# Optimization experiments

Measured on AMD Instinct MI355X. Metric: run time of the kernel, lower is better.

The kernel has to match this reference:

```python
import jax, jax.numpy as jnp
import numpy as np
import math

B, S, H, D = 4, 4096, 2048, 128  # batch, seq_len, hidden_dim, head_size

def setup_inputs() -> dict:
    key = jax.random.key(0)
    ks = jax.random.split(key, 7)
    scale = 1.0 / math.sqrt(H)
    return {
        "x": jax.random.normal(ks[0], (B, S, H), dtype=jnp.float32),
        "Wq": jax.random.normal(ks[1], (H, D), dtype=jnp.float32) * scale,
        "bq": jnp.zeros((D,), dtype=jnp.float32),
        "Wk": jax.random.normal(ks[2], (H, D), dtype=jnp.float32) * scale,
        "bk": jnp.zeros((D,), dtype=jnp.float32),
        "Wv": jax.random.normal(ks[3], (H, D), dtype=jnp.float32) * scale,
        "bv": jnp.zeros((D,), dtype=jnp.float32),
    }

def reference(x, Wq, bq, Wk, bk, Wv, bv):
    # projections: [B,S,D]
    q = x @ Wq + bq
    k = x @ Wk + bk
    v = x @ Wv + bv
    # raw scores [B,S,S] with causal mask, NO pre-softmax scaling (as in source)
    scores = jnp.einsum('bsd,btd->bst', q, k)
    causal = jnp.tril(jnp.ones((S, S), dtype=bool))
    scores = jnp.where(causal, scores, -jnp.inf)
    # non-standard: scale AFTER softmax by 1/sqrt(head_size)
    w = jax.nn.softmax(scores, axis=-1) * (1.0 / math.sqrt(D))
    # dropout p=0.0 -> identity
    return jnp.einsum('bst,btd->bsd', w, v)
```

## Files before the change

kernel.cpp:

```cpp
#include <hip/hip_runtime.h>
#include <math.h>
#include <stdint.h>

#define SEQ   4096
#define HID   2048
#define HD    128
#define NROWS 16384

typedef __attribute__((ext_vector_type(8))) short bf16x8;
typedef __attribute__((ext_vector_type(4))) float f32x4;

static constexpr float OSCALE = 0.088388347648318447f;

using gvptr = const __attribute__((address_space(1))) void*;
using lvptr = __attribute__((address_space(3))) void*;
__device__ __forceinline__ void gld_lds16(const void* g, void* l) {
    __builtin_amdgcn_global_load_lds((gvptr)g, (lvptr)l, 16, 0, 0);
}

__device__ __forceinline__ unsigned short f2bf_rne(float f) {
    union { float f; unsigned u; } v; v.f = f;
    unsigned u = v.u + 0x7fffu + ((v.u >> 16) & 1u);
    return (unsigned short)(u >> 16);
}
__device__ __forceinline__ unsigned short f2bf_tr(float f) {
    union { float f; unsigned u; } v; v.f = f;
    return (unsigned short)(v.u >> 16);
}
__device__ __forceinline__ float bf2f(unsigned short h) {
    union { unsigned u; float f; } v; v.u = ((unsigned)h) << 16;
    return v.f;
}

__global__ __launch_bounds__(256) void prep_w(
    const float* __restrict__ Wq, const float* __restrict__ Wk, const float* __restrict__ Wv,
    unsigned short* __restrict__ wth, unsigned short* __restrict__ wtl)
{
    __shared__ float T[64][68];
    const int tid = threadIdx.x;
    const int k0 = blockIdx.x * 64, n0 = blockIdx.y * 64, mm = blockIdx.z;
    const float* W = (mm == 0) ? Wq : (mm == 1) ? Wk : Wv;
    #pragma unroll
    for (int i = 0; i < 4; ++i) {
        const int fi = i * 256 + tid, kk = fi >> 4, nc = (fi & 15) * 4;
        const float4 w = *(const float4*)(W + (size_t)(k0 + kk) * HD + n0 + nc);
        T[kk][nc] = w.x; T[kk][nc + 1] = w.y; T[kk][nc + 2] = w.z; T[kk][nc + 3] = w.w;
    }
    __syncthreads();
    unsigned short* oh = wth + (size_t)mm * HD * HID;
    unsigned short* ol = wtl + (size_t)mm * HD * HID;
    #pragma unroll
    for (int i = 0; i < 4; ++i) {
        const int fi = i * 256 + tid, nn = fi >> 4, kc = (fi & 15) * 4;
        const float a = T[kc][nn], b = T[kc + 1][nn], c = T[kc + 2][nn], d = T[kc + 3][nn];
        ushort4 hv, lv;
        hv.x = f2bf_rne(a); hv.y = f2bf_rne(b); hv.z = f2bf_rne(c); hv.w = f2bf_rne(d);
        lv.x = f2bf_rne(a - bf2f(hv.x)); lv.y = f2bf_rne(b - bf2f(hv.y));
        lv.z = f2bf_rne(c - bf2f(hv.z)); lv.w = f2bf_rne(d - bf2f(hv.w));
        *(ushort4*)(oh + (size_t)(n0 + nn) * HID + k0 + kc) = hv;
        *(ushort4*)(ol + (size_t)(n0 + nn) * HID + k0 + kc) = lv;
    }
}

__global__ __launch_bounds__(256, 2) void qkv_fused(
    const float* __restrict__ x,
    const float* __restrict__ bq, const float* __restrict__ bk, const float* __restrict__ bv,
    const unsigned short* __restrict__ wth, const unsigned short* __restrict__ wtl,
    unsigned short* __restrict__ qh, unsigned short* __restrict__ ql,
    unsigned short* __restrict__ kh, unsigned short* __restrict__ kl,
    unsigned short* __restrict__ vth)
{
    __shared__ unsigned short Ah[64][72], Al[64][72];
    __shared__ unsigned short Bt[5][64][64];

    const int tid = threadIdx.x, wave = tid >> 6, lane = tid & 63;
    const int l15 = lane & 15, q4 = lane >> 4;
    const int wr = wave >> 1, wc = wave & 1;
    const int r0 = (blockIdx.x >> 1) * 64;
    const int hc = blockIdx.x & 1;

    const unsigned short* wsrc[5] = {
        wth + (size_t)hc * 64 * HID,
        wtl + (size_t)hc * 64 * HID,
        wth + (size_t)HD * HID + (size_t)hc * 64 * HID,
        wtl + (size_t)HD * HID + (size_t)hc * 64 * HID,
        wth + (size_t)2 * HD * HID + (size_t)hc * 64 * HID };

    const int srow_off = lane >> 3;
    const int schunk   = ((lane & 7) ^ (lane >> 3)) * 8;

    f32x4 accq[2][2], acck[2][2], accv[2][2];
    #pragma unroll
    for (int i = 0; i < 2; ++i)
        #pragma unroll
        for (int j = 0; j < 2; ++j) {
            accq[i][j] = (f32x4){0.f, 0.f, 0.f, 0.f};
            acck[i][j] = (f32x4){0.f, 0.f, 0.f, 0.f};
            accv[i][j] = (f32x4){0.f, 0.f, 0.f, 0.f};
        }

    const float* xbase = x + (size_t)r0 * HID;

    float4 xv[4];
    #pragma unroll
    for (int i = 0; i < 4; ++i) {
        const int fi = i * 256 + tid, row = fi >> 4, kc = (fi & 15) * 4;
        xv[i] = *(const float4*)(xbase + (size_t)row * HID + kc);
    }

    for (int k0 = 0; k0 < HID; k0 += 64) {
        __syncthreads();
        {
            #pragma unroll
            for (int a = 0; a < 5; ++a) {
                #pragma unroll
                for (int c = 0; c < 2; ++c) {
                    const int row = wave * 16 + c * 8 + srow_off;
                    gld_lds16(wsrc[a] + (size_t)row * HID + k0 + schunk,
                              &Bt[a][wave * 16 + c * 8][0]);
                }
            }
        }
        #pragma unroll
        for (int i = 0; i < 4; ++i) {
            const int fi = i * 256 + tid, row = fi >> 4, kc = (fi & 15) * 4;
            ushort4 hv, lv;
            hv.x = f2bf_tr(xv[i].x); hv.y = f2bf_tr(xv[i].y);
            hv.z = f2bf_tr(xv[i].z); hv.w = f2bf_tr(xv[i].w);
            lv.x = f2bf_tr(xv[i].x - bf2f(hv.x)); lv.y = f2bf_tr(xv[i].y - bf2f(hv.y));
            lv.z = f2bf_tr(xv[i].z - bf2f(hv.z)); lv.w = f2bf_tr(xv[i].w - bf2f(hv.w));
            *(ushort4*)&Ah[row][kc] = hv;
            *(ushort4*)&Al[row][kc] = lv;
        }
        __syncthreads();

        const int kn = (k0 + 64 < HID) ? (k0 + 64) : 0;
        #pragma unroll
        for (int i = 0; i < 4; ++i) {
            const int fi = i * 256 + tid, row = fi >> 4, kc = (fi & 15) * 4;
            xv[i] = *(const float4*)(xbase + (size_t)row * HID + kn + kc);
        }

        #pragma unroll
        for (int ks = 0; ks < 2; ++ks) {
            bf16x8 ah[2], al[2];
            #pragma unroll
            for (int mt = 0; mt < 2; ++mt) {
                ah[mt] = *(const bf16x8*)&Ah[wr * 32 + mt * 16 + l15][ks * 32 + q4 * 8];
                al[mt] = *(const bf16x8*)&Al[wr * 32 + mt * 16 + l15][ks * 32 + q4 * 8];
            }
            const int pc = ((ks * 4 + q4) ^ (l15 & 7)) * 8;
            #pragma unroll
            for (int nt = 0; nt < 2; ++nt) {
                const int br = wc * 32 + nt * 16 + l15;
                const bf16x8 qbh = *(const bf16x8*)&Bt[0][br][pc];
                const bf16x8 qbl = *(const bf16x8*)&Bt[1][br][pc];
                #pragma unroll
                for (int mt = 0; mt < 2; ++mt) {
                    accq[mt][nt] = __builtin_amdgcn_mfma_f32_16x16x32_bf16(ah[mt], qbh, accq[mt][nt], 0, 0, 0);
                    accq[mt][nt] = __builtin_amdgcn_mfma_f32_16x16x32_bf16(ah[mt], qbl, accq[mt][nt], 0, 0, 0);
                    accq[mt][nt] = __builtin_amdgcn_mfma_f32_16x16x32_bf16(al[mt], qbh, accq[mt][nt], 0, 0, 0);
                }
                const bf16x8 kbh = *(const bf16x8*)&Bt[2][br][pc];
                const bf16x8 kbl = *(const bf16x8*)&Bt[3][br][pc];
                #pragma unroll
                for (int mt = 0; mt < 2; ++mt) {
                    acck[mt][nt] = __builtin_amdgcn_mfma_f32_16x16x32_bf16(ah[mt], kbh, acck[mt][nt], 0, 0, 0);
                    acck[mt][nt] = __builtin_amdgcn_mfma_f32_16x16x32_bf16(ah[mt], kbl, acck[mt][nt], 0, 0, 0);
                    acck[mt][nt] = __builtin_amdgcn_mfma_f32_16x16x32_bf16(al[mt], kbh, acck[mt][nt], 0, 0, 0);
                }
                const bf16x8 vbh = *(const bf16x8*)&Bt[4][br][pc];
                #pragma unroll
                for (int mt = 0; mt < 2; ++mt)
                    accv[mt][nt] = __builtin_amdgcn_mfma_f32_16x16x32_bf16(ah[mt], vbh, accv[mt][nt], 0, 0, 0);
            }
        }
    }

    #pragma unroll
    for (int nt = 0; nt < 2; ++nt) {
        const int col = hc * 64 + wc * 32 + nt * 16 + l15;
        const float bbq = bq[col], bbk = bk[col], bbv = bv[col];
        #pragma unroll
        for (int mt = 0; mt < 2; ++mt) {
            const int Rb = r0 + wr * 32 + mt * 16 + q4 * 4;
            #pragma unroll
            for (int r = 0; r < 4; ++r) {
                const float vq = accq[mt][nt][r] + bbq;
                const unsigned short hq = f2bf_rne(vq);
                qh[(size_t)(Rb + r) * HD + col] = hq;
                ql[(size_t)(Rb + r) * HD + col] = f2bf_rne(vq - bf2f(hq));
                const float vk = acck[mt][nt][r] + bbk;
                const unsigned short hk = f2bf_rne(vk);
                kh[(size_t)(Rb + r) * HD + col] = hk;
                kl[(size_t)(Rb + r) * HD + col] = f2bf_rne(vk - bf2f(hk));
            }
            const int bi = Rb >> 12, s0 = Rb & 4095;
            ushort4 pv;
            pv.x = f2bf_rne(accv[mt][nt][0] + bbv);
            pv.y = f2bf_rne(accv[mt][nt][1] + bbv);
            pv.z = f2bf_rne(accv[mt][nt][2] + bbv);
            pv.w = f2bf_rne(accv[mt][nt][3] + bbv);
            *(ushort4*)(vth + ((size_t)(bi * HD + col)) * SEQ + s0) = pv;
        }
    }
}

__global__ __launch_bounds__(256, 2) void flash_mfma(
    const unsigned short* __restrict__ qh, const unsigned short* __restrict__ ql,
    const unsigned short* __restrict__ kh, const unsigned short* __restrict__ kl,
    const unsigned short* __restrict__ vth,
    unsigned short* __restrict__ oPb, float* __restrict__ mP, float* __restrict__ lP)
{
    __shared__ unsigned short Kh[64][128], Kl[64][128];
    __shared__ unsigned short Vt[128][64];
    __shared__ unsigned short Ps[4][16][72];

    const int tid = threadIdx.x, wave = tid >> 6, lane = tid & 63;
    const int l15 = lane & 15, q4 = lane >> 4;
    const int h = blockIdx.x & 3, pair = (blockIdx.x >> 2) & 31, b = blockIdx.x >> 7;

    const int krow_l = lane >> 4;
    const int vrow_l = lane >> 3;
    const int vsc = ((lane & 7) ^ (vrow_l & 7)) * 8;
    const int kkey7 = l15 & 7;
    const int vkey7 = l15 & 7;

    for (int side = 0; side < 2; ++side) {
        const int tt = side ? (63 - pair) : pair;
        const int n = tt + 1;
        const int j0 = (n * h) >> 2, j1 = (n * (h + 1)) >> 2;

        const int qrow = b * SEQ + tt * 64 + wave * 16 + l15;
        bf16x8 aqh[4], aql[4];
        #pragma unroll
        for (int ks = 0; ks < 4; ++ks) {
            aqh[ks] = *(const bf16x8*)(qh + (size_t)qrow * HD + ks * 32 + q4 * 8);
            aql[ks] = *(const bf16x8*)(ql + (size_t)qrow * HD + ks * 32 + q4 * 8);
        }
        f32x4 oa[8];
        #pragma unroll
        for (int d = 0; d < 8; ++d) oa[d] = (f32x4){0.f, 0.f, 0.f, 0.f};
        float m_r[4] = {-INFINITY, -INFINITY, -INFINITY, -INFINITY};
        float l_r[4] = {0.f, 0.f, 0.f, 0.f};

        for (int j = j0; j < j1; ++j) {
            __syncthreads();
            {
                const size_t kb = (size_t)b * SEQ + j * 64;
                #pragma unroll
                for (int c = 0; c < 4; ++c) {
                    const int rl = c * 4 + krow_l;
                    const int sc = (l15 ^ (rl & 7)) * 8;
                    const size_t gr = (kb + wave * 16 + rl) * HD + sc;
                    gld_lds16(kh + gr, &Kh[wave * 16 + c * 4][0]);
                    gld_lds16(kl + gr, &Kl[wave * 16 + c * 4][0]);
                }
                #pragma unroll
                for (int c = 0; c < 4; ++c)
                    gld_lds16(vth + ((size_t)(b * HD + wave * 32 + c * 8 + vrow_l)) * SEQ
                                  + j * 64 + vsc,
                              &Vt[wave * 32 + c * 8][0]);
            }
            __syncthreads();

            f32x4 s[4];
            #pragma unroll
            for (int nt = 0; nt < 4; ++nt) s[nt] = (f32x4){0.f, 0.f, 0.f, 0.f};
            #pragma unroll
            for (int ks = 0; ks < 4; ++ks) {
                const int pc = ((ks * 4 + q4) ^ kkey7) * 8;
                #pragma unroll
                for (int nt = 0; nt < 4; ++nt) {
                    const bf16x8 bh = *(const bf16x8*)&Kh[nt * 16 + l15][pc];
                    const bf16x8 bl = *(const bf16x8*)&Kl[nt * 16 + l15][pc];
                    s[nt] = __builtin_amdgcn_mfma_f32_16x16x32_bf16(aqh[ks], bh, s[nt], 0, 0, 0);
                    s[nt] = __builtin_amdgcn_mfma_f32_16x16x32_bf16(aql[ks], bh, s[nt], 0, 0, 0);
                    s[nt] = __builtin_amdgcn_mfma_f32_16x16x32_bf16(aqh[ks], bl, s[nt], 0, 0, 0);
                }
            }
            if (j == tt) {
                #pragma unroll
                for (int nt = 0; nt < 4; ++nt) {
                    const int cl = nt * 16 + l15;
                    #pragma unroll
                    for (int r = 0; r < 4; ++r) {
                        const int rl = wave * 16 + q4 * 4 + r;
                        if (cl > rl) s[nt][r] = -INFINITY;
                    }
                }
            }
            #pragma unroll
            for (int r = 0; r < 4; ++r) {
                float mt = fmaxf(fmaxf(s[0][r], s[1][r]), fmaxf(s[2][r], s[3][r]));
                mt = fmaxf(mt, __shfl_xor(mt, 1));
                mt = fmaxf(mt, __shfl_xor(mt, 2));
                mt = fmaxf(mt, __shfl_xor(mt, 4));
                mt = fmaxf(mt, __shfl_xor(mt, 8));
                const float mn = fmaxf(m_r[r], mt);
                const float al = __expf(m_r[r] - mn);
                m_r[r] = mn;
                const float p0 = __expf(s[0][r] - mn), p1 = __expf(s[1][r] - mn);
                const float p2 = __expf(s[2][r] - mn), p3 = __expf(s[3][r] - mn);
                Ps[wave][q4 * 4 + r][l15]      = f2bf_tr(p0);
                Ps[wave][q4 * 4 + r][16 + l15] = f2bf_tr(p1);
                Ps[wave][q4 * 4 + r][32 + l15] = f2bf_tr(p2);
                Ps[wave][q4 * 4 + r][48 + l15] = f2bf_tr(p3);
                float ps = p0 + p1 + p2 + p3;
                ps += __shfl_xor(ps, 1); ps += __shfl_xor(ps, 2);
                ps += __shfl_xor(ps, 4); ps += __shfl_xor(ps, 8);
                l_r[r] = l_r[r] * al + ps;
                #pragma unroll
                for (int d = 0; d < 8; ++d) oa[d][r] *= al;
            }
            const bf16x8 ap0 = *(const bf16x8*)&Ps[wave][l15][q4 * 8];
            const bf16x8 ap1 = *(const bf16x8*)&Ps[wave][l15][32 + q4 * 8];
            #pragma unroll
            for (int d = 0; d < 8; ++d) {
                const bf16x8 bv0 = *(const bf16x8*)&Vt[d * 16 + l15][(q4 ^ vkey7) * 8];
                const bf16x8 bv1 = *(const bf16x8*)&Vt[d * 16 + l15][((4 + q4) ^ vkey7) * 8];
                oa[d] = __builtin_amdgcn_mfma_f32_16x16x32_bf16(ap0, bv0, oa[d], 0, 0, 0);
                oa[d] = __builtin_amdgcn_mfma_f32_16x16x32_bf16(ap1, bv1, oa[d], 0, 0, 0);
            }
        }

        const int R0 = b * SEQ + tt * 64 + wave * 16 + q4 * 4;
        unsigned short* op = oPb + (size_t)h * NROWS * HD;
        #pragma unroll
        for (int d = 0; d < 8; ++d)
            #pragma unroll
            for (int r = 0; r < 4; ++r)
                op[(size_t)(R0 + r) * HD + d * 16 + l15] = f2bf_rne(oa[d][r]);
        if (l15 == 0) {
            #pragma unroll
            for (int r = 0; r < 4; ++r) {
                mP[h * NROWS + R0 + r] = m_r[r];
                lP[h * NROWS + R0 + r] = l_r[r];
            }
        }
    }
}

__global__ __launch_bounds__(256) void flash_merge(
    const unsigned short* __restrict__ oPb, const float* __restrict__ mP,
    const float* __restrict__ lP, float* __restrict__ out)
{
    const int idx = blockIdx.x * 256 + threadIdx.x;
    const int r = idx >> 5, c = (idx & 31) * 4;
    float m[4], l[4];
    #pragma unroll
    for (int i = 0; i < 4; ++i) { m[i] = mP[i * NROWS + r]; l[i] = lP[i * NROWS + r]; }
    float M = fmaxf(fmaxf(m[0], m[1]), fmaxf(m[2], m[3]));
    float a[4], lsum = 0.f;
    #pragma unroll
    for (int i = 0; i < 4; ++i) { a[i] = __expf(m[i] - M); lsum += l[i] * a[i]; }
    const float inv = OSCALE / lsum;
    float ox = 0.f, oy = 0.f, oz = 0.f, ow = 0.f;
    #pragma unroll
    for (int i = 0; i < 4; ++i) {
        const ushort4 ov = *(const ushort4*)(oPb + (size_t)i * NROWS * HD + (size_t)r * HD + c);
        ox += a[i] * bf2f(ov.x); oy += a[i] * bf2f(ov.y);
        oz += a[i] * bf2f(ov.z); ow += a[i] * bf2f(ov.w);
    }
    float4 o; o.x = ox * inv; o.y = oy * inv; o.z = oz * inv; o.w = ow * inv;
    *(float4*)(out + (size_t)r * HD + c) = o;
}

extern "C" void kernel_launch(void* const* d_in, const int* in_sizes, int n_in,
                              void* d_out, int out_size, void* d_ws, size_t ws_size,
                              hipStream_t stream)
{
    (void)in_sizes; (void)n_in; (void)out_size; (void)ws_size;
    const float* x  = (const float*)d_in[0];
    const float* Wq = (const float*)d_in[1];
    const float* bq = (const float*)d_in[2];
    const float* Wk = (const float*)d_in[3];
    const float* bk = (const float*)d_in[4];
    const float* Wv = (const float*)d_in[5];
    const float* bv = (const float*)d_in[6];
    float* out = (float*)d_out;

    char* w = (char*)d_ws;
    unsigned short* qh  = (unsigned short*)(w);
    unsigned short* ql  = (unsigned short*)(w + 4194304);
    unsigned short* kh  = (unsigned short*)(w + 8388608);
    unsigned short* kl  = (unsigned short*)(w + 12582912);
    unsigned short* vth = (unsigned short*)(w + 16777216);
    unsigned short* wth = (unsigned short*)(w + 20971520);
    unsigned short* wtl = (unsigned short*)(w + 22544384);
    unsigned short* oPb = (unsigned short*)(w + 24117248);
    float* mP = (float*)(w + 40894464);
    float* lP = (float*)(w + 41156608);

    prep_w<<<dim3(32, 2, 3), 256, 0, stream>>>(Wq, Wk, Wv, wth, wtl);
    qkv_fused<<<512, 256, 0, stream>>>(x, bq, bk, bv, wth, wtl, qh, ql, kh, kl, vth);
    flash_mfma<<<512, 256, 0, stream>>>(qh, ql, kh, kl, vth, oPb, mP, lP);
    flash_merge<<<2048, 256, 0, stream>>>(oPb, mP, lP, out);
}
```

Before: 320.7 us.

## Load QKV weight fragments directly into registers and retile waves by column

The QKV projection kernel no longer stages the five weight tiles through shared memory with global_load_lds. Each wave now owns a 16-column slice across all 64 rows and loads its B fragments straight from global memory into registers. The A fragments are still read from shared memory for four row tiles. This removes the LDS weight buffer and the LDS reads of B, which frees shared memory and may raise occupancy. In exchange, the per-lane global loads are strided by HID with no coalescing across lanes, and each wave now issues more A-fragment LDS reads.

Result: slower. 339.2 us (+5.8%).

```diff
diff --git a/kernel.cpp b/kernel.cpp
--- a/kernel.cpp
+++ b/kernel.cpp
@@ -71,33 +71,27 @@
     unsigned short* __restrict__ vth)
 {
     __shared__ unsigned short Ah[64][72], Al[64][72];
-    __shared__ unsigned short Bt[5][64][64];
 
     const int tid = threadIdx.x, wave = tid >> 6, lane = tid & 63;
     const int l15 = lane & 15, q4 = lane >> 4;
-    const int wr = wave >> 1, wc = wave & 1;
     const int r0 = (blockIdx.x >> 1) * 64;
     const int hc = blockIdx.x & 1;
 
-    const unsigned short* wsrc[5] = {
-        wth + (size_t)hc * 64 * HID,
-        wtl + (size_t)hc * 64 * HID,
-        wth + (size_t)HD * HID + (size_t)hc * 64 * HID,
-        wtl + (size_t)HD * HID + (size_t)hc * 64 * HID,
-        wth + (size_t)2 * HD * HID + (size_t)hc * 64 * HID };
-
-    const int srow_off = lane >> 3;
-    const int schunk   = ((lane & 7) ^ (lane >> 3)) * 8;
-
-    f32x4 accq[2][2], acck[2][2], accv[2][2];
-    #pragma unroll
-    for (int i = 0; i < 2; ++i)
-        #pragma unroll
-        for (int j = 0; j < 2; ++j) {
-            accq[i][j] = (f32x4){0.f, 0.f, 0.f, 0.f};
-            acck[i][j] = (f32x4){0.f, 0.f, 0.f, 0.f};
-            accv[i][j] = (f32x4){0.f, 0.f, 0.f, 0.f};
-        }
+    const int col = hc * 64 + wave * 16 + l15;
+    const unsigned short* pQh = wth + (size_t)col * HID;
+    const unsigned short* pQl = wtl + (size_t)col * HID;
+    const unsigned short* pKh = pQh + (size_t)HD * HID;
+    const unsigned short* pKl = pQl + (size_t)HD * HID;
+    const unsigned short* pVh = pKh + (size_t)HD * HID;
+    const int kq = q4 * 8;
+
+    f32x4 accq[4], acck[4], accv[4];
+    #pragma unroll
+    for (int mt = 0; mt < 4; ++mt) {
+        accq[mt] = (f32x4){0.f, 0.f, 0.f, 0.f};
+        acck[mt] = (f32x4){0.f, 0.f, 0.f, 0.f};
+        accv[mt] = (f32x4){0.f, 0.f, 0.f, 0.f};
+    }
 
     const float* xbase = x + (size_t)r0 * HID;
 
@@ -110,17 +104,18 @@
 
     for (int k0 = 0; k0 < HID; k0 += 64) {
         __syncthreads();
-        {
-            #pragma unroll
-            for (int a = 0; a < 5; ++a) {
-                #pragma unroll
-                for (int c = 0; c < 2; ++c) {
-                    const int row = wave * 16 + c * 8 + srow_off;
-                    gld_lds16(wsrc[a] + (size_t)row * HID + k0 + schunk,
-                              &Bt[a][wave * 16 + c * 8][0]);
-                }
-            }
-        }
+
+        const bf16x8 b0qh = *(const bf16x8*)(pQh + k0 + kq);
+        const bf16x8 b0ql = *(const bf16x8*)(pQl + k0 + kq);
+        const bf16x8 b0kh = *(const bf16x8*)(pKh + k0 + kq);
+        const bf16x8 b0kl = *(const bf16x8*)(pKl + k0 + kq);
+        const bf16x8 b0vh = *(const bf16x8*)(pVh + k0 + kq);
+        const bf16x8 b1qh = *(const bf16x8*)(pQh + k0 + 32 + kq);
+        const bf16x8 b1ql = *(const bf16x8*)(pQl + k0 + 32 + kq);
+        const bf16x8 b1kh = *(const bf16x8*)(pKh + k0 + 32 + kq);
+        const bf16x8 b1kl = *(const bf16x8*)(pKl + k0 + 32 + kq);
+        const bf16x8 b1vh = *(const bf16x8*)(pVh + k0 + 32 + kq);
+
         #pragma unroll
         for (int i = 0; i < 4; ++i) {
             const int fi = i * 256 + tid, row = fi >> 4, kc = (fi & 15) * 4;
@@ -141,68 +136,61 @@
             xv[i] = *(const float4*)(xbase + (size_t)row * HID + kn + kc);
         }
 
-        #pragma unroll
-        for (int ks = 0; ks < 2; ++ks) {
-            bf16x8 ah[2], al[2];
-            #pragma unroll
-            for (int mt = 0; mt < 2; ++mt) {
-                ah[mt] = *(const bf16x8*)&Ah[wr * 32 + mt * 16 + l15][ks * 32 + q4 * 8];
-                al[mt] = *(const bf16x8*)&Al[wr * 32 + mt * 16 + l15][ks * 32 + q4 * 8];
-            }
-            const int pc = ((ks * 4 + q4) ^ (l15 & 7)) * 8;
-            #pragma unroll
-            for (int nt = 0; nt < 2; ++nt) {
-                const int br = wc * 32 + nt * 16 + l15;
-                const bf16x8 qbh = *(const bf16x8*)&Bt[0][br][pc];
-                const bf16x8 qbl = *(const bf16x8*)&Bt[1][br][pc];
-                #pragma unroll
-                for (int mt = 0; mt < 2; ++mt) {
-                    accq[mt][nt] = __builtin_amdgcn_mfma_f32_16x16x32_bf16(ah[mt], qbh, accq[mt][nt], 0, 0, 0);
-                    accq[mt][nt] = __builtin_amdgcn_mfma_f32_16x16x32_bf16(ah[mt], qbl, accq[mt][nt], 0, 0, 0);
-                    accq[mt][nt] = __builtin_amdgcn_mfma_f32_16x16x32_bf16(al[mt], qbh, accq[mt][nt], 0, 0, 0);
-                }
-                const bf16x8 kbh = *(const bf16x8*)&Bt[2][br][pc];
-                const bf16x8 kbl = *(const bf16x8*)&Bt[3][br][pc];
-                #pragma unroll
-                for (int mt = 0; mt < 2; ++mt) {
-                    acck[mt][nt] = __builtin_amdgcn_mfma_f32_16x16x32_bf16(ah[mt], kbh, acck[mt][nt], 0, 0, 0);
-                    acck[mt][nt] = __builtin_amdgcn_mfma_f32_16x16x32_bf16(ah[mt], kbl, acck[mt][nt], 0, 0, 0);
-                    acck[mt][nt] = __builtin_amdgcn_mfma_f32_16x16x32_bf16(al[mt], kbh, acck[mt][nt], 0, 0, 0);
-                }
-                const bf16x8 vbh = *(const bf16x8*)&Bt[4][br][pc];
-                #pragma unroll
-                for (int mt = 0; mt < 2; ++mt)
-                    accv[mt][nt] = __builtin_amdgcn_mfma_f32_16x16x32_bf16(ah[mt], vbh, accv[mt][nt], 0, 0, 0);
-            }
-        }
-    }
-
-    #pragma unroll
-    for (int nt = 0; nt < 2; ++nt) {
-        const int col = hc * 64 + wc * 32 + nt * 16 + l15;
-        const float bbq = bq[col], bbk = bk[col], bbv = bv[col];
-        #pragma unroll
-        for (int mt = 0; mt < 2; ++mt) {
-            const int Rb = r0 + wr * 32 + mt * 16 + q4 * 4;
-            #pragma unroll
-            for (int r = 0; r < 4; ++r) {
-                const float vq = accq[mt][nt][r] + bbq;
-                const unsigned short hq = f2bf_rne(vq);
-                qh[(size_t)(Rb + r) * HD + col] = hq;
-                ql[(size_t)(Rb + r) * HD + col] = f2bf_rne(vq - bf2f(hq));
-                const float vk = acck[mt][nt][r] + bbk;
-                const unsigned short hk = f2bf_rne(vk);
-                kh[(size_t)(Rb + r) * HD + col] = hk;
-                kl[(size_t)(Rb + r) * HD + col] = f2bf_rne(vk - bf2f(hk));
-            }
-            const int bi = Rb >> 12, s0 = Rb & 4095;
-            ushort4 pv;
-            pv.x = f2bf_rne(accv[mt][nt][0] + bbv);
-            pv.y = f2bf_rne(accv[mt][nt][1] + bbv);
-            pv.z = f2bf_rne(accv[mt][nt][2] + bbv);
-            pv.w = f2bf_rne(accv[mt][nt][3] + bbv);
-            *(ushort4*)(vth + ((size_t)(bi * HD + col)) * SEQ + s0) = pv;
-        }
+        bf16x8 ah[4], al[4];
+        #pragma unroll
+        for (int mt = 0; mt < 4; ++mt) {
+            ah[mt] = *(const bf16x8*)&Ah[mt * 16 + l15][kq];
+            al[mt] = *(const bf16x8*)&Al[mt * 16 + l15][kq];
+        }
+        #pragma unroll
+        for (int mt = 0; mt < 4; ++mt) {
+            accq[mt] = __builtin_amdgcn_mfma_f32_16x16x32_bf16(ah[mt], b0qh, accq[mt], 0, 0, 0);
+            accq[mt] = __builtin_amdgcn_mfma_f32_16x16x32_bf16(ah[mt], b0ql, accq[mt], 0, 0, 0);
+            accq[mt] = __builtin_amdgcn_mfma_f32_16x16x32_bf16(al[mt], b0qh, accq[mt], 0, 0, 0);
+            acck[mt] = __builtin_amdgcn_mfma_f32_16x16x32_bf16(ah[mt], b0kh, acck[mt], 0, 0, 0);
+            acck[mt] = __builtin_amdgcn_mfma_f32_16x16x32_bf16(ah[mt], b0kl, acck[mt], 0, 0, 0);
+            acck[mt] = __builtin_amdgcn_mfma_f32_16x16x32_bf16(al[mt], b0kh, acck[mt], 0, 0, 0);
+            accv[mt] = __builtin_amdgcn_mfma_f32_16x16x32_bf16(ah[mt], b0vh, accv[mt], 0, 0, 0);
+        }
+        #pragma unroll
+        for (int mt = 0; mt < 4; ++mt) {
+            ah[mt] = *(const bf16x8*)&Ah[mt * 16 + l15][32 + kq];
+            al[mt] = *(const bf16x8*)&Al[mt * 16 + l15][32 + kq];
+        }
+        #pragma unroll
+        for (int mt = 0; mt < 4; ++mt) {
+            accq[mt] = __builtin_amdgcn_mfma_f32_16x16x32_bf16(ah[mt], b1qh, accq[mt], 0, 0, 0);
+            accq[mt] = __builtin_amdgcn_mfma_f32_16x16x32_bf16(ah[mt], b1ql, accq[mt], 0, 0, 0);
+            accq[mt] = __builtin_amdgcn_mfma_f32_16x16x32_bf16(al[mt], b1qh, accq[mt], 0, 0, 0);
+            acck[mt] = __builtin_amdgcn_mfma_f32_16x16x32_bf16(ah[mt], b1kh, acck[mt], 0, 0, 0);
+            acck[mt] = __builtin_amdgcn_mfma_f32_16x16x32_bf16(ah[mt], b1kl, acck[mt], 0, 0, 0);
+            acck[mt] = __builtin_amdgcn_mfma_f32_16x16x32_bf16(al[mt], b1kh, acck[mt], 0, 0, 0);
+            accv[mt] = __builtin_amdgcn_mfma_f32_16x16x32_bf16(ah[mt], b1vh, accv[mt], 0, 0, 0);
+        }
+    }
+
+    const float bbq = bq[col], bbk = bk[col], bbv = bv[col];
+    #pragma unroll
+    for (int mt = 0; mt < 4; ++mt) {
+        const int Rb = r0 + mt * 16 + q4 * 4;
+        #pragma unroll
+        for (int r = 0; r < 4; ++r) {
+            const float vq = accq[mt][r] + bbq;
+            const unsigned short hqv = f2bf_rne(vq);
+            qh[(size_t)(Rb + r) * HD + col] = hqv;
+            ql[(size_t)(Rb + r) * HD + col] = f2bf_rne(vq - bf2f(hqv));
+            const float vk = acck[mt][r] + bbk;
+            const unsigned short hkv = f2bf_rne(vk);
+            kh[(size_t)(Rb + r) * HD + col] = hkv;
+            kl[(size_t)(Rb + r) * HD + col] = f2bf_rne(vk - bf2f(hkv));
+        }
+        const int bi = Rb >> 12, s0 = Rb & 4095;
+        ushort4 pv;
+        pv.x = f2bf_rne(accv[mt][0] + bbv);
+        pv.y = f2bf_rne(accv[mt][1] + bbv);
+        pv.z = f2bf_rne(accv[mt][2] + bbv);
+        pv.w = f2bf_rne(accv[mt][3] + bbv);
+        *(ushort4*)(vth + ((size_t)(bi * HD + col)) * SEQ + s0) = pv;
     }
 }
 
```

## Split QKV projection into per-matrix blocks with full head width

Applied to the files above, without the earlier changes.

Replaces the fused QKV kernel, which computed half the head columns of Q, K and V together per block, with a kernel where each block computes all 128 columns of a single projection (Q, K or V) for a 64-row tile, launching 768 blocks. V blocks skip the low-part split of x and weights, so they do a third of the MFMA work and LDS loads of Q/K blocks. The x tile in LDS now uses an XOR swizzle instead of padding, and launch bounds ask for three blocks per CU. The trade-off is that each x tile is now read and converted by three blocks instead of two, and the uneven block costs may leave the load unbalanced.

Result: faster. 311.4 us (-2.9%).

```diff
diff --git a/kernel.cpp b/kernel.cpp
--- a/kernel.cpp
+++ b/kernel.cpp
@@ -62,7 +62,7 @@
     }
 }
 
-__global__ __launch_bounds__(256, 2) void qkv_fused(
+__global__ __launch_bounds__(256, 3) void qkv_split(
     const float* __restrict__ x,
     const float* __restrict__ bq, const float* __restrict__ bk, const float* __restrict__ bv,
     const unsigned short* __restrict__ wth, const unsigned short* __restrict__ wtl,
@@ -70,34 +70,29 @@
     unsigned short* __restrict__ kh, unsigned short* __restrict__ kl,
     unsigned short* __restrict__ vth)
 {
-    __shared__ unsigned short Ah[64][72], Al[64][72];
-    __shared__ unsigned short Bt[5][64][64];
+    __shared__ unsigned short Ah[64][64], Al[64][64];
+    __shared__ unsigned short Bh[128][64], Bl[128][64];
 
     const int tid = threadIdx.x, wave = tid >> 6, lane = tid & 63;
     const int l15 = lane & 15, q4 = lane >> 4;
     const int wr = wave >> 1, wc = wave & 1;
-    const int r0 = (blockIdx.x >> 1) * 64;
-    const int hc = blockIdx.x & 1;
-
-    const unsigned short* wsrc[5] = {
-        wth + (size_t)hc * 64 * HID,
-        wtl + (size_t)hc * 64 * HID,
-        wth + (size_t)HD * HID + (size_t)hc * 64 * HID,
-        wtl + (size_t)HD * HID + (size_t)hc * 64 * HID,
-        wth + (size_t)2 * HD * HID + (size_t)hc * 64 * HID };
-
-    const int srow_off = lane >> 3;
-    const int schunk   = ((lane & 7) ^ (lane >> 3)) * 8;
-
-    f32x4 accq[2][2], acck[2][2], accv[2][2];
-    #pragma unroll
-    for (int i = 0; i < 2; ++i)
-        #pragma unroll
-        for (int j = 0; j < 2; ++j) {
-            accq[i][j] = (f32x4){0.f, 0.f, 0.f, 0.f};
-            acck[i][j] = (f32x4){0.f, 0.f, 0.f, 0.f};
-            accv[i][j] = (f32x4){0.f, 0.f, 0.f, 0.f};
-        }
+    const int type = blockIdx.x % 3;
+    const int tile = blockIdx.x / 3;
+    const int r0 = tile * 64;
+    const bool qk = (type < 2);
+
+    const unsigned short* wh = wth + (size_t)type * HD * HID;
+    const unsigned short* wl = wtl + (size_t)type * HD * HID;
+
+    const int srow   = lane >> 3;
+    const int schunk = ((lane & 7) ^ srow) * 8;
+
+    f32x4 acc[2][4];
+    #pragma unroll
+    for (int mt = 0; mt < 2; ++mt)
+        #pragma unroll
+        for (int nt = 0; nt < 4; ++nt)
+            acc[mt][nt] = (f32x4){0.f, 0.f, 0.f, 0.f};
 
     const float* xbase = x + (size_t)r0 * HID;
 
@@ -110,27 +105,35 @@
 
     for (int k0 = 0; k0 < HID; k0 += 64) {
         __syncthreads();
+
         {
             #pragma unroll
-            for (int a = 0; a < 5; ++a) {
-                #pragma unroll
-                for (int c = 0; c < 2; ++c) {
-                    const int row = wave * 16 + c * 8 + srow_off;
-                    gld_lds16(wsrc[a] + (size_t)row * HID + k0 + schunk,
-                              &Bt[a][wave * 16 + c * 8][0]);
+            for (int c = 0; c < 4; ++c) {
+                const int row = wave * 32 + c * 8;
+                gld_lds16(wh + (size_t)(row + srow) * HID + k0 + schunk, &Bh[row][0]);
+            }
+            if (qk) {
+                #pragma unroll
+                for (int c = 0; c < 4; ++c) {
+                    const int row = wave * 32 + c * 8;
+                    gld_lds16(wl + (size_t)(row + srow) * HID + k0 + schunk, &Bl[row][0]);
                 }
             }
         }
         #pragma unroll
         for (int i = 0; i < 4; ++i) {
             const int fi = i * 256 + tid, row = fi >> 4, kc = (fi & 15) * 4;
-            ushort4 hv, lv;
+            const int pk = ((kc >> 3) ^ (row & 7)) * 8 + (kc & 7);
+            ushort4 hv;
             hv.x = f2bf_tr(xv[i].x); hv.y = f2bf_tr(xv[i].y);
             hv.z = f2bf_tr(xv[i].z); hv.w = f2bf_tr(xv[i].w);
-            lv.x = f2bf_tr(xv[i].x - bf2f(hv.x)); lv.y = f2bf_tr(xv[i].y - bf2f(hv.y));
-            lv.z = f2bf_tr(xv[i].z - bf2f(hv.z)); lv.w = f2bf_tr(xv[i].w - bf2f(hv.w));
-            *(ushort4*)&Ah[row][kc] = hv;
-            *(ushort4*)&Al[row][kc] = lv;
+            *(ushort4*)&Ah[row][pk] = hv;
+            if (qk) {
+                ushort4 lv;
+                lv.x = f2bf_tr(xv[i].x - bf2f(hv.x)); lv.y = f2bf_tr(xv[i].y - bf2f(hv.y));
+                lv.z = f2bf_tr(xv[i].z - bf2f(hv.z)); lv.w = f2bf_tr(xv[i].w - bf2f(hv.w));
+                *(ushort4*)&Al[row][pk] = lv;
+            }
         }
         __syncthreads();
 
@@ -143,65 +146,69 @@
 
         #pragma unroll
         for (int ks = 0; ks < 2; ++ks) {
+            const int pc = ((ks * 4 + q4) ^ (l15 & 7)) * 8;
             bf16x8 ah[2], al[2];
             #pragma unroll
             for (int mt = 0; mt < 2; ++mt) {
-                ah[mt] = *(const bf16x8*)&Ah[wr * 32 + mt * 16 + l15][ks * 32 + q4 * 8];
-                al[mt] = *(const bf16x8*)&Al[wr * 32 + mt * 16 + l15][ks * 32 + q4 * 8];
-            }
-            const int pc = ((ks * 4 + q4) ^ (l15 & 7)) * 8;
-            #pragma unroll
-            for (int nt = 0; nt < 2; ++nt) {
-                const int br = wc * 32 + nt * 16 + l15;
-                const bf16x8 qbh = *(const bf16x8*)&Bt[0][br][pc];
-                const bf16x8 qbl = *(const bf16x8*)&Bt[1][br][pc];
-                #pragma unroll
-                for (int mt = 0; mt < 2; ++mt) {
-                    accq[mt][nt] = __builtin_amdgcn_mfma_f32_16x16x32_bf16(ah[mt], qbh, accq[mt][nt], 0, 0, 0);
-                    accq[mt][nt] = __builtin_amdgcn_mfma_f32_16x16x32_bf16(ah[mt], qbl, accq[mt][nt], 0, 0, 0);
-                    accq[mt][nt] = __builtin_amdgcn_mfma_f32_16x16x32_bf16(al[mt], qbh, accq[mt][nt], 0, 0, 0);
-                }
-                const bf16x8 kbh = *(const bf16x8*)&Bt[2][br][pc];
-                const bf16x8 kbl = *(const bf16x8*)&Bt[3][br][pc];
-                #pragma unroll
-                for (int mt = 0; mt < 2; ++mt) {
-                    acck[mt][nt] = __builtin_amdgcn_mfma_f32_16x16x32_bf16(ah[mt], kbh, acck[mt][nt], 0, 0, 0);
-                    acck[mt][nt] = __builtin_amdgcn_mfma_f32_16x16x32_bf16(ah[mt], kbl, acck[mt][nt], 0, 0, 0);
-                    acck[mt][nt] = __builtin_amdgcn_mfma_f32_16x16x32_bf16(al[mt], kbh, acck[mt][nt], 0, 0, 0);
-                }
-                const bf16x8 vbh = *(const bf16x8*)&Bt[4][br][pc];
+                const int ar = wr * 32 + mt * 16 + l15;
+                ah[mt] = *(const bf16x8*)&Ah[ar][pc];
+                if (qk) al[mt] = *(const bf16x8*)&Al[ar][pc];
+            }
+            #pragma unroll
+            for (int nt = 0; nt < 4; ++nt) {
+                const int br = wc * 64 + nt * 16 + l15;
+                const bf16x8 bh = *(const bf16x8*)&Bh[br][pc];
                 #pragma unroll
                 for (int mt = 0; mt < 2; ++mt)
-                    accv[mt][nt] = __builtin_amdgcn_mfma_f32_16x16x32_bf16(ah[mt], vbh, accv[mt][nt], 0, 0, 0);
-            }
-        }
-    }
-
-    #pragma unroll
-    for (int nt = 0; nt < 2; ++nt) {
-        const int col = hc * 64 + wc * 32 + nt * 16 + l15;
-        const float bbq = bq[col], bbk = bk[col], bbv = bv[col];
-        #pragma unroll
-        for (int mt = 0; mt < 2; ++mt) {
-            const int Rb = r0 + wr * 32 + mt * 16 + q4 * 4;
-            #pragma unroll
-            for (int r = 0; r < 4; ++r) {
-                const float vq = accq[mt][nt][r] + bbq;
-                const unsigned short hq = f2bf_rne(vq);
-                qh[(size_t)(Rb + r) * HD + col] = hq;
-                ql[(size_t)(Rb + r) * HD + col] = f2bf_rne(vq - bf2f(hq));
-                const float vk = acck[mt][nt][r] + bbk;
-                const unsigned short hk = f2bf_rne(vk);
-                kh[(size_t)(Rb + r) * HD + col] = hk;
-                kl[(size_t)(Rb + r) * HD + col] = f2bf_rne(vk - bf2f(hk));
-            }
-            const int bi = Rb >> 12, s0 = Rb & 4095;
-            ushort4 pv;
-            pv.x = f2bf_rne(accv[mt][nt][0] + bbv);
-            pv.y = f2bf_rne(accv[mt][nt][1] + bbv);
-            pv.z = f2bf_rne(accv[mt][nt][2] + bbv);
-            pv.w = f2bf_rne(accv[mt][nt][3] + bbv);
-            *(ushort4*)(vth + ((size_t)(bi * HD + col)) * SEQ + s0) = pv;
+                    acc[mt][nt] = __builtin_amdgcn_mfma_f32_16x16x32_bf16(ah[mt], bh, acc[mt][nt], 0, 0, 0);
+                if (qk) {
+                    const bf16x8 bl = *(const bf16x8*)&Bl[br][pc];
+                    #pragma unroll
+                    for (int mt = 0; mt < 2; ++mt) {
+                        acc[mt][nt] = __builtin_amdgcn_mfma_f32_16x16x32_bf16(ah[mt], bl, acc[mt][nt], 0, 0, 0);
+                        acc[mt][nt] = __builtin_amdgcn_mfma_f32_16x16x32_bf16(al[mt], bh, acc[mt][nt], 0, 0, 0);
+                    }
+                }
+            }
+        }
+    }
+
+    if (qk) {
+        const float* bb = (type == 0) ? bq : bk;
+        unsigned short* oh = (type == 0) ? qh : kh;
+        unsigned short* ol = (type == 0) ? ql : kl;
+        #pragma unroll
+        for (int nt = 0; nt < 4; ++nt) {
+            const int col = wc * 64 + nt * 16 + l15;
+            const float bias = bb[col];
+            #pragma unroll
+            for (int mt = 0; mt < 2; ++mt) {
+                const int Rb = r0 + wr * 32 + mt * 16 + q4 * 4;
+                #pragma unroll
+                for (int r = 0; r < 4; ++r) {
+                    const float v = acc[mt][nt][r] + bias;
+                    const unsigned short h = f2bf_rne(v);
+                    oh[(size_t)(Rb + r) * HD + col] = h;
+                    ol[(size_t)(Rb + r) * HD + col] = f2bf_rne(v - bf2f(h));
+                }
+            }
+        }
+    } else {
+        #pragma unroll
+        for (int nt = 0; nt < 4; ++nt) {
+            const int col = wc * 64 + nt * 16 + l15;
+            const float bias = bv[col];
+            #pragma unroll
+            for (int mt = 0; mt < 2; ++mt) {
+                const int Rb = r0 + wr * 32 + mt * 16 + q4 * 4;
+                const int bi = Rb >> 12, s0 = Rb & 4095;
+                ushort4 pv;
+                pv.x = f2bf_rne(acc[mt][nt][0] + bias);
+                pv.y = f2bf_rne(acc[mt][nt][1] + bias);
+                pv.z = f2bf_rne(acc[mt][nt][2] + bias);
+                pv.w = f2bf_rne(acc[mt][nt][3] + bias);
+                *(ushort4*)(vth + ((size_t)(bi * HD + col)) * SEQ + s0) = pv;
+            }
         }
     }
 }
@@ -393,7 +400,7 @@
     float* lP = (float*)(w + 41156608);
 
     prep_w<<<dim3(32, 2, 3), 256, 0, stream>>>(Wq, Wk, Wv, wth, wtl);
-    qkv_fused<<<512, 256, 0, stream>>>(x, bq, bk, bv, wth, wtl, qh, ql, kh, kl, vth);
+    qkv_split<<<768, 256, 0, stream>>>(x, bq, bk, bv, wth, wtl, qh, ql, kh, kl, vth);
     flash_mfma<<<512, 256, 0, stream>>>(qh, ql, kh, kl, vth, oPb, mP, lP);
     flash_merge<<<2048, 256, 0, stream>>>(oPb, mP, lP, out);
 }
```
